# Performance work log

Hardware: AMD Instinct MI355X
Metric: run time of the kernel (lower is better)

## Reference

```python
import jax, jax.numpy as jnp
import numpy as np

B, S, D, H = 4, 2048, 256, 8
HD = D // H
SCALE = float(np.sqrt(HD))  # temperature = head_dim ** 0.5


def setup_inputs() -> dict:
    key = jax.random.key(0)
    ks = jax.random.split(key, 12)
    w = lambda k, shape: jax.random.normal(k, shape, dtype=jnp.float32) * 0.05
    x = jax.random.normal(ks[0], (B, S, D), dtype=jnp.float32)
    adj = jax.random.randint(ks[1], (B, S, S), 0, 2, dtype=jnp.int32)
    return {
        "x": x,
        "adj": adj,
        "w_qkv": w(ks[2], (3 * D, D)),
        "b_qkv": jnp.zeros((3 * D,), jnp.float32),
        "ln_g": jnp.ones((D,), jnp.float32),
        "ln_b": jnp.zeros((D,), jnp.float32),
        "w_fc": w(ks[3], (D, D)),
        "b_fc": jnp.zeros((D,), jnp.float32),
        "w_z": w(ks[4], (D, D)),
        "b_z": jnp.full((D,), -2.0, jnp.float32),  # init_bias fills w_z bias with -2
        "u_z": w(ks[5], (D, D)),
        "w_r": w(ks[6], (D, D)),
        "u_r": w(ks[7], (D, D)),
        "w_g": w(ks[8], (D, D)),
        "u_g": w(ks[9], (D, D)),
    }


def reference(x, adj, w_qkv, b_qkv, ln_g, ln_b, w_fc, b_fc,
              w_z, b_z, u_z, w_r, u_r, w_g, u_g):
    residual = x
    # LayerNorm (eps=1e-5, torch default)
    mu = jnp.mean(x, axis=-1, keepdims=True)
    var = jnp.var(x, axis=-1, keepdims=True)
    xn = (x - mu) / jnp.sqrt(var + 1e-5) * ln_g + ln_b
    # fused QKV projection -> (B*H, S, 3*HD), batch-major over (b, h)
    qkv = xn @ w_qkv.T + b_qkv                       # [B,S,3D]
    qkv = qkv.reshape(B, S, H, 3 * HD).transpose(0, 2, 1, 3).reshape(B * H, S, 3 * HD)
    q, k, v = jnp.split(qkv, 3, axis=-1)
    # masked scaled dot-product attention (full NxN scores, as in original)
    attn = jnp.einsum('nqd,nkd->nqk', q, k) / SCALE  # [B*H,S,S]
    adj_r = jnp.repeat(adj, H, axis=0)               # batch-major, matches attn layout
    attn = jnp.where(adj_r == 0, -jnp.inf, attn)
    attn = jax.nn.softmax(attn, axis=-1)
    out = jnp.einsum('nqk,nkd->nqd', attn, v)        # [B*H,S,HD]
    # Faithful replication of torch's view(n_head, batch, ...) applied to
    # batch-major data (an ordering quirk in the original module).
    out = out.reshape(H, B, S, HD).transpose(1, 2, 0, 3).reshape(B, S, D)
    y = jax.nn.relu(out @ w_fc.T + b_fc)
    # GRU gate: x=residual, y=attention branch
    z = jax.nn.sigmoid(y @ w_z.T + b_z + residual @ u_z.T)
    r = jax.nn.sigmoid(y @ w_r.T + residual @ u_r.T)
    h_hat = jnp.tanh(y @ w_g.T + (r * residual) @ u_g.T)
    return (1.0 - z) * residual + z * h_hat
```

## Files before the change

### kernel.cpp

```cpp
#include <hip/hip_runtime.h>
#include <hip/hip_bf16.h>
#include <math.h>

#define B_  4
#define S_  2048
#define D_  256
#define H_  8
#define HD_ 32
#define QSCALE 0.25504175929589786f

typedef short  bf16x8 __attribute__((ext_vector_type(8)));
typedef float  f32x4  __attribute__((ext_vector_type(4)));
typedef float  f32x16 __attribute__((ext_vector_type(16)));
typedef unsigned short ushort_t;
typedef unsigned int   uint_t;

__device__ __forceinline__ ushort_t f2b(float f) {
    union { float f; unsigned u; } v; v.f = f;
    unsigned r = (v.u + 0x7FFFu + ((v.u >> 16) & 1u)) >> 16;
    return (ushort_t)r;
}
__device__ __forceinline__ float b2f(ushort_t s) {
    return __uint_as_float((uint_t)s << 16);
}
__device__ __forceinline__ f32x16 zero16() {
    f32x16 z;
#pragma unroll
    for (int i = 0; i < 16; ++i) z[i] = 0.f;
    return z;
}

__device__ __forceinline__ float wave_sum(float v) {
#pragma unroll
    for (int o = 32; o > 0; o >>= 1) v += __shfl_down(v, o, 64);
    return v;
}
__device__ __forceinline__ float block_sum256(float v, float* scr) {
    v = wave_sum(v);
    int lane = threadIdx.x & 63, wid = threadIdx.x >> 6;
    if (lane == 0) scr[wid] = v;
    __syncthreads();
    float r = scr[0] + scr[1] + scr[2] + scr[3];
    __syncthreads();
    return r;
}

#define WQ_SZ 196608
#define WS_SZ 65536
#define NB_ADJ 8192
#define NB_WC  2560
#define NB_LN  8192
__global__ __launch_bounds__(256)
void prep_kernel(const int* __restrict__ adj, uint_t* __restrict__ bits,
                 const float* __restrict__ w0, const float* __restrict__ w1,
                 const float* __restrict__ w2, const float* __restrict__ w3,
                 const float* __restrict__ w4, const float* __restrict__ w5,
                 const float* __restrict__ w6, const float* __restrict__ w7,
                 ushort_t* __restrict__ wout,
                 const float* __restrict__ x, const float* __restrict__ g,
                 const float* __restrict__ bb, ushort_t* __restrict__ xn_b) {
    __shared__ float scr[4];
    int blk = blockIdx.x, tid = threadIdx.x;
    if (blk < NB_ADJ) {
        int lane = tid & 63;
#pragma unroll
        for (int gp = 0; gp < 8; ++gp) {
            size_t i = ((size_t)blk * 8 + gp) * 256 + tid;
            unsigned long long m = __ballot(adj[i] != 0);
            size_t wbase = (((size_t)blk * 8 + gp) * 256 + (tid & ~63)) >> 5;
            if (lane == 0)  bits[wbase]     = (uint_t)m;
            if (lane == 32) bits[wbase + 1] = (uint_t)(m >> 32);
        }
    } else if (blk < NB_ADJ + NB_WC) {
        int idx = (blk - NB_ADJ) * 256 + tid;
        const float* src; int o;
        if (idx < WQ_SZ) { src = w0; o = idx; }
        else {
            int j = idx - WQ_SZ, seg = j >> 16; o = j & (WS_SZ - 1);
            src = (seg == 0) ? w1 : (seg == 1) ? w2 : (seg == 2) ? w3 :
                  (seg == 3) ? w4 : (seg == 4) ? w5 : (seg == 5) ? w6 : w7;
        }
        int j  = o & 7;
        int l  = (o >> 3) & 15;
        int qd = (o >> 7) & 3;
        int ks = (o >> 9) & 7;
        int ct = o >> 12;
        wout[idx] = f2b(src[(ct * 16 + l) * 256 + ks * 32 + qd * 8 + j]);
    } else {
        size_t base = (size_t)(blk - NB_ADJ - NB_WC) * D_;
        float v  = x[base + tid];
        float mu = block_sum256(v, scr) * (1.0f / D_);
        float d  = v - mu;
        float var = block_sum256(d * d, scr) * (1.0f / D_);
        float rstd = rsqrtf(var + 1e-5f);
        xn_b[base + tid] = f2b(d * rstd * g[tid] + bb[tid]);
    }
}

__global__ __launch_bounds__(256)
void gemm_qkv(const ushort_t* __restrict__ A, const ushort_t* __restrict__ Wf,
              const float* __restrict__ bias, ushort_t* __restrict__ outb,
              ushort_t* __restrict__ vT) {
    __shared__ ushort_t Sa[64][264];
    int tid = threadIdx.x;
    int wave = tid >> 6, lane = tid & 63, l = lane & 15, quad = lane >> 4;
    int wm = wave >> 1, wn = wave & 1;
    int m0 = blockIdx.y * 64, n0 = blockIdx.x * 64;
    {
        int row = tid >> 2, c0 = (tid & 3) * 64;
        const ushort_t* ap = A + (size_t)(m0 + row) * 256 + c0;
#pragma unroll
        for (int j = 0; j < 8; ++j)
            *(uint4*)&Sa[row][c0 + 8 * j] = ((const uint4*)ap)[j];
    }
    __syncthreads();

    bf16x8 af[2][8];
#pragma unroll
    for (int mt = 0; mt < 2; ++mt)
#pragma unroll
        for (int ks = 0; ks < 8; ++ks)
            af[mt][ks] = *(const bf16x8*)&Sa[wm * 32 + mt * 16 + l][ks * 32 + quad * 8];

    f32x4 acc[2][2];
#pragma unroll
    for (int i = 0; i < 2; ++i)
#pragma unroll
        for (int j = 0; j < 2; ++j) acc[i][j] = (f32x4){0.f, 0.f, 0.f, 0.f};

#pragma unroll
    for (int nt = 0; nt < 2; ++nt) {
        int ct = (n0 >> 4) + wn * 2 + nt;
        bf16x8 wfr[8];
#pragma unroll
        for (int ks = 0; ks < 8; ++ks)
            wfr[ks] = *(const bf16x8*)(Wf + (((size_t)ct * 8 + ks) * 64 + lane) * 8);
#pragma unroll
        for (int ks = 0; ks < 8; ++ks) {
            acc[0][nt] = __builtin_amdgcn_mfma_f32_16x16x32_bf16(af[0][ks], wfr[ks], acc[0][nt], 0, 0, 0);
            acc[1][nt] = __builtin_amdgcn_mfma_f32_16x16x32_bf16(af[1][ks], wfr[ks], acc[1][nt], 0, 0, 0);
        }
    }

    __syncthreads();
    ushort_t* So = &Sa[0][0];
#pragma unroll
    for (int nt = 0; nt < 2; ++nt) {
        int col = wn * 32 + nt * 16 + l;
        int gcol = n0 + col;
        float bv = bias[gcol];
        float qs = ((gcol % 96) < 32) ? QSCALE : 1.0f;
#pragma unroll
        for (int mt = 0; mt < 2; ++mt)
#pragma unroll
            for (int r = 0; r < 4; ++r) {
                int row = wm * 32 + mt * 16 + quad * 4 + r;
                So[row * 72 + col] = f2b((acc[mt][nt][r] + bv) * qs);
            }
    }
    __syncthreads();
    {
        int row = tid >> 2, seg = tid & 3;
        uint4 v0 = *(uint4*)&So[row * 72 + seg * 16];
        uint4 v1 = *(uint4*)&So[row * 72 + seg * 16 + 8];
        ushort_t* op = outb + (size_t)(m0 + row) * 768 + n0 + seg * 16;
        ((uint4*)op)[0] = v0;
        ((uint4*)op)[1] = v1;
    }

    int vs = n0 % 96;
    if (vs != 0) {
        int vloc = (vs == 64) ? 0 : 32;
        int h  = (n0 + vloc) / 96;
        int b  = m0 >> 11;
        int s0 = m0 & (S_ - 1);
        ushort_t* vstage = &Sa[0][0] + 8192;
        {
            int c = tid & 31, seg = tid >> 5;
            ushort_t tmp[8];
#pragma unroll
            for (int i = 0; i < 8; ++i)
                tmp[i] = So[(seg * 8 + i) * 72 + vloc + c];
            uint_t u[4];
#pragma unroll
            for (int i = 0; i < 4; ++i)
                u[i] = (uint_t)tmp[2 * i] | ((uint_t)tmp[2 * i + 1] << 16);
            *(uint4*)&vstage[c * 72 + seg * 8] = make_uint4(u[0], u[1], u[2], u[3]);
        }
        __syncthreads();
        {
            int d = tid >> 3, tseg = tid & 7;
            uint4 v = *(uint4*)&vstage[d * 72 + tseg * 8];
            *(uint4*)&vT[((size_t)(b * 8 + h) * 32 + d) * S_ + s0 + tseg * 8] = v;
        }
    }
}

__global__ __launch_bounds__(256)
void fused_gate(const ushort_t* __restrict__ attn_b, const float* __restrict__ xf,
                const ushort_t* __restrict__ wfc, const ushort_t* __restrict__ wz,
                const ushort_t* __restrict__ uz, const ushort_t* __restrict__ wr,
                const ushort_t* __restrict__ ur, const ushort_t* __restrict__ wg,
                const ushort_t* __restrict__ ug, const float* __restrict__ bfc,
                const float* __restrict__ bz, float* __restrict__ out) {
    __shared__ ushort_t Sa[16][264];
    __shared__ ushort_t Sx[16][264];
    __shared__ ushort_t Sy[16][264];
    __shared__ ushort_t St[16][264];
    int tid = threadIdx.x;
    int wave = tid >> 6, lane = tid & 63, l = lane & 15, quad = lane >> 4;
    int m0 = blockIdx.x * 16;
    int colbase = wave * 64;

    {
        int row = tid >> 4, c0 = (tid & 15) * 16;
        const ushort_t* ap = attn_b + (size_t)(m0 + row) * 256 + c0;
        uint4 a0 = ((const uint4*)ap)[0];
        uint4 a1 = ((const uint4*)ap)[1];
        *(uint4*)&Sa[row][c0] = a0;
        *(uint4*)&Sa[row][c0 + 8] = a1;
        const float4* xp = (const float4*)(xf + (size_t)(m0 + row) * 256 + c0);
        float4 f0 = xp[0], f1 = xp[1], f2_ = xp[2], f3 = xp[3];
        union { __hip_bfloat162 h[4]; uint4 u; } p0, p1;
        p0.h[0] = __float22bfloat162_rn(make_float2(f0.x, f0.y));
        p0.h[1] = __float22bfloat162_rn(make_float2(f0.z, f0.w));
        p0.h[2] = __float22bfloat162_rn(make_float2(f1.x, f1.y));
        p0.h[3] = __float22bfloat162_rn(make_float2(f1.z, f1.w));
        p1.h[0] = __float22bfloat162_rn(make_float2(f2_.x, f2_.y));
        p1.h[1] = __float22bfloat162_rn(make_float2(f2_.z, f2_.w));
        p1.h[2] = __float22bfloat162_rn(make_float2(f3.x, f3.y));
        p1.h[3] = __float22bfloat162_rn(make_float2(f3.z, f3.w));
        *(uint4*)&Sx[row][c0]     = p0.u;
        *(uint4*)&Sx[row][c0 + 8] = p1.u;
    }
    __syncthreads();

    {
        bf16x8 af[8];
#pragma unroll
        for (int ks = 0; ks < 8; ++ks)
            af[ks] = *(const bf16x8*)&Sa[l][ks * 32 + quad * 8];
        f32x4 ya[4];
#pragma unroll
        for (int nt = 0; nt < 4; ++nt) ya[nt] = (f32x4){0.f, 0.f, 0.f, 0.f};
#pragma unroll
        for (int nt = 0; nt < 4; ++nt) {
            size_t fb = ((size_t)(wave * 4 + nt) * 8) * 512 + lane * 8;
#pragma unroll
            for (int ks = 0; ks < 8; ++ks) {
                bf16x8 wfr = *(const bf16x8*)(wfc + fb + ks * 512);
                ya[nt] = __builtin_amdgcn_mfma_f32_16x16x32_bf16(af[ks], wfr, ya[nt], 0, 0, 0);
            }
        }
#pragma unroll
        for (int nt = 0; nt < 4; ++nt) {
            int col = colbase + nt * 16 + l;
            float bv = bfc[col];
#pragma unroll
            for (int r = 0; r < 4; ++r)
                Sy[quad * 4 + r][col] = f2b(fmaxf(ya[nt][r] + bv, 0.0f));
        }
    }
    __syncthreads();

    f32x4 az[4], ar[4], ag[4];
#pragma unroll
    for (int nt = 0; nt < 4; ++nt) {
        az[nt] = (f32x4){0.f, 0.f, 0.f, 0.f};
        ar[nt] = (f32x4){0.f, 0.f, 0.f, 0.f};
        ag[nt] = (f32x4){0.f, 0.f, 0.f, 0.f};
    }
#pragma unroll
    for (int nt = 0; nt < 4; ++nt) {
        size_t fb = ((size_t)(wave * 4 + nt) * 8) * 512 + lane * 8;
#pragma unroll
        for (int ks = 0; ks < 8; ++ks) {
            bf16x8 fy = *(const bf16x8*)&Sy[l][ks * 32 + quad * 8];
            bf16x8 fx = *(const bf16x8*)&Sx[l][ks * 32 + quad * 8];
            bf16x8 fz  = *(const bf16x8*)(wz + fb + ks * 512);
            bf16x8 fuz = *(const bf16x8*)(uz + fb + ks * 512);
            bf16x8 fr  = *(const bf16x8*)(wr + fb + ks * 512);
            bf16x8 fur = *(const bf16x8*)(ur + fb + ks * 512);
            bf16x8 fg  = *(const bf16x8*)(wg + fb + ks * 512);
            az[nt] = __builtin_amdgcn_mfma_f32_16x16x32_bf16(fy, fz,  az[nt], 0, 0, 0);
            az[nt] = __builtin_amdgcn_mfma_f32_16x16x32_bf16(fx, fuz, az[nt], 0, 0, 0);
            ar[nt] = __builtin_amdgcn_mfma_f32_16x16x32_bf16(fy, fr,  ar[nt], 0, 0, 0);
            ar[nt] = __builtin_amdgcn_mfma_f32_16x16x32_bf16(fx, fur, ar[nt], 0, 0, 0);
            ag[nt] = __builtin_amdgcn_mfma_f32_16x16x32_bf16(fy, fg,  ag[nt], 0, 0, 0);
        }
    }
#pragma unroll
    for (int nt = 0; nt < 4; ++nt) {
        int col = colbase + nt * 16 + l;
        float bzv = bz[col];
#pragma unroll
        for (int r = 0; r < 4; ++r) {
            int row = quad * 4 + r;
            az[nt][r] = 1.0f / (1.0f + __expf(-(az[nt][r] + bzv)));
            float rr  = 1.0f / (1.0f + __expf(-ar[nt][r]));
            St[row][col] = f2b(rr * b2f(Sx[row][col]));
        }
    }
    __syncthreads();

    f32x4 fcc[4];
#pragma unroll
    for (int nt = 0; nt < 4; ++nt) fcc[nt] = (f32x4){0.f, 0.f, 0.f, 0.f};
#pragma unroll
    for (int nt = 0; nt < 4; ++nt) {
        size_t fb = ((size_t)(wave * 4 + nt) * 8) * 512 + lane * 8;
#pragma unroll
        for (int ks = 0; ks < 8; ++ks) {
            bf16x8 ft = *(const bf16x8*)&St[l][ks * 32 + quad * 8];
            bf16x8 fu = *(const bf16x8*)(ug + fb + ks * 512);
            fcc[nt] = __builtin_amdgcn_mfma_f32_16x16x32_bf16(ft, fu, fcc[nt], 0, 0, 0);
        }
    }
#pragma unroll
    for (int nt = 0; nt < 4; ++nt) {
        int col = colbase + nt * 16 + l;
#pragma unroll
        for (int r = 0; r < 4; ++r) {
            int row = quad * 4 + r;
            float v = ag[nt][r] + fcc[nt][r];
            float e = __expf(2.0f * v);
            float h = 1.0f - 2.0f / (e + 1.0f);
            float zz = az[nt][r];
            size_t idx = (size_t)(m0 + row) * 256 + col;
            out[idx] = (1.0f - zz) * xf[idx] + zz * h;
        }
    }
}

__global__ __launch_bounds__(256)
void attn_kernel(const ushort_t* __restrict__ qkvb, const ushort_t* __restrict__ vT,
                 const uint_t* __restrict__ abits, ushort_t* __restrict__ attn_b) {
    __shared__ ushort_t Ks[2][64][40];
    __shared__ ushort_t Vt[2][32][72];

    int tid = threadIdx.x;
    int wave = tid >> 6, lane = tid & 63;
    int lane5 = lane & 31, hi = lane >> 5;
    int hsh8 = hi * 8;

    int lid = blockIdx.y * 16 + blockIdx.x;
    int L   = (lid & 7) * 64 + (lid >> 3);
    int q0  = (L & 15) * 128;
    int n   = L >> 4;
    int b = n >> 3, h = n & 7;
    int bp = n & 3, hp = n >> 2;

    const ushort_t* base = qkvb + (size_t)b * S_ * 768 + h * 96;
    int qbase = wave * 32;
    int myq = q0 + qbase + lane5;

    bf16x8 qf1 = *(const bf16x8*)(base + (size_t)myq * 768 + hsh8);
    bf16x8 qf2 = *(const bf16x8*)(base + (size_t)myq * 768 + 16 + hsh8);

    bf16x8 ones;
#pragma unroll
    for (int i = 0; i < 8; ++i) ones[i] = (short)0x3F80;

    f32x16 oacc = zero16(), aones = zero16();

    int skey = tid >> 2, spart = tid & 3;
    int prow = (skey & ~12) | ((skey & 4) << 1) | ((skey & 8) >> 1);
    int kcol = (spart * 8) ^ (((prow >> 3) & 1) << 3);
    int vd = tid >> 3, vk = (tid & 7) * 8;
    const ushort_t* vptr = vT + ((size_t)n * 32 + vd) * S_ + vk;
    const uint_t* aptr = abits + ((size_t)b * S_ + myq) * 64;

    uint2 aw = *(const uint2*)aptr;
    {
        uint4 k0v = *(const uint4*)(base + (size_t)skey * 768 + 32 + spart * 8);
        uint4 v0v = *(const uint4*)(vptr);
        *(uint4*)&Ks[0][prow][kcol] = k0v;
        *(uint4*)&Vt[0][vd][vk] = v0v;
    }
    uint4 kv = *(const uint4*)(base + (size_t)(64 + skey) * 768 + 32 + spart * 8);
    uint4 vv = *(const uint4*)(vptr + 64);
    __syncthreads();

    int b3 = (lane >> 3) & 1;

    for (int k0 = 0; k0 < S_; k0 += 64) {
        int cur = (k0 >> 6) & 1;
        bool more = (k0 + 64 < S_);
        uint2 awn;
        if (more) {
            *(uint4*)&Ks[cur ^ 1][prow][kcol] = kv;
            *(uint4*)&Vt[cur ^ 1][vd][vk] = vv;
            awn = *(const uint2*)(aptr + ((k0 + 64) >> 5));
            if (k0 + 128 < S_) {
                kv = *(const uint4*)(base + (size_t)(k0 + 128 + skey) * 768 + 32 + spart * 8);
                vv = *(const uint4*)(vptr + k0 + 128);
            }
        }
        uint_t awx = aw.x, awy = aw.y;

#pragma unroll
        for (int kb2 = 0; kb2 < 2; ++kb2) {
            const int kb = kb2 * 32;
            bf16x8 kf1 = *(const bf16x8*)&Ks[cur][kb + lane5][(hi ^ b3) * 8];
            bf16x8 kf2 = *(const bf16x8*)&Ks[cur][kb + lane5][((2 + hi) ^ b3) * 8];
            f32x16 sc = zero16();
            sc = __builtin_amdgcn_mfma_f32_32x32x16_bf16(kf1, qf1, sc, 0, 0, 0);
            sc = __builtin_amdgcn_mfma_f32_32x32x16_bf16(kf2, qf2, sc, 0, 0, 0);

            uint_t wsub = (kb2 ? awy : awx) >> hsh8;
            union { uint_t u[8]; bf16x8 v[2]; } pp;
#pragma unroll
            for (int i = 0; i < 8; ++i) {
                const int c = 2 * i + ((i >> 2) * 8);
                float e0 = exp2f(sc[2 * i]);
                float e1 = exp2f(sc[2 * i + 1]);
                uint_t m0 = (uint_t)((int)(wsub << (31 - c)) >> 31);
                uint_t m1 = (uint_t)((int)(wsub << (30 - c)) >> 31);
                e0 = __uint_as_float(__float_as_uint(e0) & m0);
                e1 = __uint_as_float(__float_as_uint(e1) & m1);
                union { __hip_bfloat162 b2; uint_t u; } p;
                p.b2 = __float22bfloat162_rn(make_float2(e0, e1));
                pp.u[i] = p.u;
            }

            bf16x8 vb1 = *(const bf16x8*)&Vt[cur][lane5][kb + hsh8];
            bf16x8 vb2 = *(const bf16x8*)&Vt[cur][lane5][kb + 16 + hsh8];

            __builtin_amdgcn_s_setprio(1);
            oacc  = __builtin_amdgcn_mfma_f32_32x32x16_bf16(pp.v[0], vb1,  oacc,  0, 0, 0);
            aones = __builtin_amdgcn_mfma_f32_32x32x16_bf16(pp.v[0], ones, aones, 0, 0, 0);
            oacc  = __builtin_amdgcn_mfma_f32_32x32x16_bf16(pp.v[1], vb2,  oacc,  0, 0, 0);
            aones = __builtin_amdgcn_mfma_f32_32x32x16_bf16(pp.v[1], ones, aones, 0, 0, 0);
            __builtin_amdgcn_s_setprio(0);
        }

        if (more) aw = awn;
        __syncthreads();
    }

    ushort_t* Ost = &Ks[0][0][0];
#pragma unroll
    for (int r = 0; r < 16; ++r) {
        int qr = (r & 3) + 8 * (r >> 2) + 4 * hi;
        Ost[(qbase + qr) * 40 + lane5] = f2b(oacc[r] / aones[r]);
    }
    __syncthreads();
#pragma unroll
    for (int bt = 0; bt < 2; ++bt) {
        int row = (tid >> 2) + bt * 64;
        int part = tid & 3;
        uint4 v = *(uint4*)&Ost[row * 40 + part * 8];
        *(uint4*)&attn_b[((size_t)(bp * S_ + q0 + row)) * 256 + hp * 32 + part * 8] = v;
    }
}

extern "C" void kernel_launch(void* const* d_in, const int* in_sizes, int n_in,
                              void* d_out, int out_size, void* d_ws, size_t ws_size,
                              hipStream_t stream) {
    const float* x     = (const float*)d_in[0];
    const int*   adj   = (const int*)d_in[1];
    const float* w_qkv = (const float*)d_in[2];
    const float* b_qkv = (const float*)d_in[3];
    const float* ln_g  = (const float*)d_in[4];
    const float* ln_b  = (const float*)d_in[5];
    const float* w_fc  = (const float*)d_in[6];
    const float* b_fc  = (const float*)d_in[7];
    const float* w_z   = (const float*)d_in[8];
    const float* b_z   = (const float*)d_in[9];
    const float* u_z   = (const float*)d_in[10];
    const float* w_r   = (const float*)d_in[11];
    const float* u_r   = (const float*)d_in[12];
    const float* w_g   = (const float*)d_in[13];
    const float* u_g   = (const float*)d_in[14];
    float* out = (float*)d_out;

    const size_t TOK  = (size_t)B_ * S_;
    const size_t TOKD = TOK * D_;
    ushort_t* xn_b   = (ushort_t*)d_ws;
    ushort_t* qkv_b  = xn_b + TOKD;
    ushort_t* attn_b = qkv_b + TOK * 768;
    ushort_t* wb     = attn_b + TOKD;
    uint_t*   bits   = (uint_t*)(wb + WQ_SZ + 7 * WS_SZ);
    ushort_t* vTb    = (ushort_t*)(bits + (size_t)B_ * S_ * S_ / 32);

    ushort_t* wq_b  = wb;
    ushort_t* wfc_b = wb + WQ_SZ;
    ushort_t* wz_b  = wfc_b + WS_SZ;
    ushort_t* uz_b  = wz_b + WS_SZ;
    ushort_t* wr_b  = uz_b + WS_SZ;
    ushort_t* ur_b  = wr_b + WS_SZ;
    ushort_t* wg_b  = ur_b + WS_SZ;
    ushort_t* ug_b  = wg_b + WS_SZ;

    prep_kernel<<<NB_ADJ + NB_WC + NB_LN, 256, 0, stream>>>(
        adj, bits, w_qkv, w_fc, w_z, u_z, w_r, u_r, w_g, u_g, wb,
        x, ln_g, ln_b, xn_b);

    gemm_qkv<<<dim3(12, 128), 256, 0, stream>>>(xn_b, wq_b, b_qkv, qkv_b, vTb);

    attn_kernel<<<dim3(S_ / 128, B_ * H_), 256, 0, stream>>>(qkv_b, vTb, bits, attn_b);

    fused_gate<<<512, 256, 0, stream>>>(
        attn_b, x, wfc_b, wz_b, uz_b, wr_b, ur_b, wg_b, ug_b, b_fc, b_z, out);
}
```

Before: 235.9 us.

## Split key tile across wave pairs in attention and reduce partial accumulators

The attention kernel now gives each block 64 queries instead of 128 and doubles the grid. Each pair of waves shares a 32-query tile, and each wave in the pair handles one 32-key half of every 64-key tile. The two partial output and denominator accumulators are summed through shared memory at the end. This raises parallelism and occupancy and shortens each wave's serial loop, at the cost of K/V tiles being loaded once per 64 queries instead of per 128, plus an extra LDS reduction with barriers.

```diff
diff --git a/kernel.cpp b/kernel.cpp
--- a/kernel.cpp
+++ b/kernel.cpp
@@ -342,17 +342,19 @@
     int wave = tid >> 6, lane = tid & 63;
     int lane5 = lane & 31, hi = lane >> 5;
     int hsh8 = hi * 8;
-
-    int lid = blockIdx.y * 16 + blockIdx.x;
-    int L   = (lid & 7) * 64 + (lid >> 3);
-    int q0  = (L & 15) * 128;
-    int n   = L >> 4;
+    int pair = wave >> 1, half = wave & 1;
+
+    int lid = blockIdx.y * 32 + blockIdx.x;
+    int L   = (lid & 7) * 128 + (lid >> 3);
+    int q0  = (L & 31) * 64;
+    int n   = L >> 5;
     int b = n >> 3, h = n & 7;
     int bp = n & 3, hp = n >> 2;
 
     const ushort_t* base = qkvb + (size_t)b * S_ * 768 + h * 96;
-    int qbase = wave * 32;
+    int qbase = pair * 32;
     int myq = q0 + qbase + lane5;
+    const int kb = half * 32;
 
     bf16x8 qf1 = *(const bf16x8*)(base + (size_t)myq * 768 + hsh8);
     bf16x8 qf2 = *(const bf16x8*)(base + (size_t)myq * 768 + 16 + hsh8);
@@ -368,9 +370,9 @@
     int kcol = (spart * 8) ^ (((prow >> 3) & 1) << 3);
     int vd = tid >> 3, vk = (tid & 7) * 8;
     const ushort_t* vptr = vT + ((size_t)n * 32 + vd) * S_ + vk;
-    const uint_t* aptr = abits + ((size_t)b * S_ + myq) * 64;
-
-    uint2 aw = *(const uint2*)aptr;
+    const uint_t* aptr = abits + ((size_t)b * S_ + myq) * 64 + half;
+
+    uint_t aw = aptr[0];
     {
         uint4 k0v = *(const uint4*)(base + (size_t)skey * 768 + 32 + spart * 8);
         uint4 v0v = *(const uint4*)(vptr);
@@ -386,69 +388,100 @@
     for (int k0 = 0; k0 < S_; k0 += 64) {
         int cur = (k0 >> 6) & 1;
         bool more = (k0 + 64 < S_);
-        uint2 awn;
+        uint_t awn;
         if (more) {
             *(uint4*)&Ks[cur ^ 1][prow][kcol] = kv;
             *(uint4*)&Vt[cur ^ 1][vd][vk] = vv;
-            awn = *(const uint2*)(aptr + ((k0 + 64) >> 5));
+            awn = aptr[(k0 + 64) >> 5];
             if (k0 + 128 < S_) {
                 kv = *(const uint4*)(base + (size_t)(k0 + 128 + skey) * 768 + 32 + spart * 8);
                 vv = *(const uint4*)(vptr + k0 + 128);
             }
         }
-        uint_t awx = aw.x, awy = aw.y;
-
-#pragma unroll
-        for (int kb2 = 0; kb2 < 2; ++kb2) {
-            const int kb = kb2 * 32;
-            bf16x8 kf1 = *(const bf16x8*)&Ks[cur][kb + lane5][(hi ^ b3) * 8];
-            bf16x8 kf2 = *(const bf16x8*)&Ks[cur][kb + lane5][((2 + hi) ^ b3) * 8];
-            f32x16 sc = zero16();
-            sc = __builtin_amdgcn_mfma_f32_32x32x16_bf16(kf1, qf1, sc, 0, 0, 0);
-            sc = __builtin_amdgcn_mfma_f32_32x32x16_bf16(kf2, qf2, sc, 0, 0, 0);
-
-            uint_t wsub = (kb2 ? awy : awx) >> hsh8;
-            union { uint_t u[8]; bf16x8 v[2]; } pp;
-#pragma unroll
-            for (int i = 0; i < 8; ++i) {
-                const int c = 2 * i + ((i >> 2) * 8);
-                float e0 = exp2f(sc[2 * i]);
-                float e1 = exp2f(sc[2 * i + 1]);
-                uint_t m0 = (uint_t)((int)(wsub << (31 - c)) >> 31);
-                uint_t m1 = (uint_t)((int)(wsub << (30 - c)) >> 31);
-                e0 = __uint_as_float(__float_as_uint(e0) & m0);
-                e1 = __uint_as_float(__float_as_uint(e1) & m1);
-                union { __hip_bfloat162 b2; uint_t u; } p;
-                p.b2 = __float22bfloat162_rn(make_float2(e0, e1));
-                pp.u[i] = p.u;
-            }
-
-            bf16x8 vb1 = *(const bf16x8*)&Vt[cur][lane5][kb + hsh8];
-            bf16x8 vb2 = *(const bf16x8*)&Vt[cur][lane5][kb + 16 + hsh8];
-
-            __builtin_amdgcn_s_setprio(1);
-            oacc  = __builtin_amdgcn_mfma_f32_32x32x16_bf16(pp.v[0], vb1,  oacc,  0, 0, 0);
-            aones = __builtin_amdgcn_mfma_f32_32x32x16_bf16(pp.v[0], ones, aones, 0, 0, 0);
-            oacc  = __builtin_amdgcn_mfma_f32_32x32x16_bf16(pp.v[1], vb2,  oacc,  0, 0, 0);
-            aones = __builtin_amdgcn_mfma_f32_32x32x16_bf16(pp.v[1], ones, aones, 0, 0, 0);
-            __builtin_amdgcn_s_setprio(0);
-        }
+
+        bf16x8 kf1 = *(const bf16x8*)&Ks[cur][kb + lane5][(hi ^ b3) * 8];
+        bf16x8 kf2 = *(const bf16x8*)&Ks[cur][kb + lane5][((2 + hi) ^ b3) * 8];
+        f32x16 sc = zero16();
+        sc = __builtin_amdgcn_mfma_f32_32x32x16_bf16(kf1, qf1, sc, 0, 0, 0);
+        sc = __builtin_amdgcn_mfma_f32_32x32x16_bf16(kf2, qf2, sc, 0, 0, 0);
+
+        uint_t wsub = aw >> hsh8;
+        union { uint_t u[8]; bf16x8 v[2]; } pp;
+#pragma unroll
+        for (int i = 0; i < 8; ++i) {
+            const int c = 2 * i + ((i >> 2) * 8);
+            float e0 = exp2f(sc[2 * i]);
+            float e1 = exp2f(sc[2 * i + 1]);
+            uint_t m0 = (uint_t)((int)(wsub << (31 - c)) >> 31);
+            uint_t m1 = (uint_t)((int)(wsub << (30 - c)) >> 31);
+            e0 = __uint_as_float(__float_as_uint(e0) & m0);
+            e1 = __uint_as_float(__float_as_uint(e1) & m1);
+            union { __hip_bfloat162 b2; uint_t u; } p;
+            p.b2 = __float22bfloat162_rn(make_float2(e0, e1));
+            pp.u[i] = p.u;
+        }
+
+        bf16x8 vb1 = *(const bf16x8*)&Vt[cur][lane5][kb + hsh8];
+        bf16x8 vb2 = *(const bf16x8*)&Vt[cur][lane5][kb + 16 + hsh8];
+
+        __builtin_amdgcn_s_setprio(1);
+        oacc  = __builtin_amdgcn_mfma_f32_32x32x16_bf16(pp.v[0], vb1,  oacc,  0, 0, 0);
+        aones = __builtin_amdgcn_mfma_f32_32x32x16_bf16(pp.v[0], ones, aones, 0, 0, 0);
+        oacc  = __builtin_amdgcn_mfma_f32_32x32x16_bf16(pp.v[1], vb2,  oacc,  0, 0, 0);
+        aones = __builtin_amdgcn_mfma_f32_32x32x16_bf16(pp.v[1], ones, aones, 0, 0, 0);
+        __builtin_amdgcn_s_setprio(0);
 
         if (more) aw = awn;
         __syncthreads();
     }
 
+    float* red = (float*)&Ks[0][0][0];
+    if (half) {
+        float* dst = red + pair * 2048 + lane * 4;
+#pragma unroll
+        for (int j = 0; j < 4; ++j) {
+            f32x4 t;
+            t[0] = oacc[4 * j]; t[1] = oacc[4 * j + 1];
+            t[2] = oacc[4 * j + 2]; t[3] = oacc[4 * j + 3];
+            *(f32x4*)(dst + j * 256) = t;
+        }
+#pragma unroll
+        for (int j = 0; j < 4; ++j) {
+            f32x4 t;
+            t[0] = aones[4 * j]; t[1] = aones[4 * j + 1];
+            t[2] = aones[4 * j + 2]; t[3] = aones[4 * j + 3];
+            *(f32x4*)(dst + (4 + j) * 256) = t;
+        }
+    }
+    __syncthreads();
+    if (!half) {
+        const float* src = red + pair * 2048 + lane * 4;
+#pragma unroll
+        for (int j = 0; j < 4; ++j) {
+            f32x4 t = *(const f32x4*)(src + j * 256);
+            oacc[4 * j] += t[0]; oacc[4 * j + 1] += t[1];
+            oacc[4 * j + 2] += t[2]; oacc[4 * j + 3] += t[3];
+        }
+#pragma unroll
+        for (int j = 0; j < 4; ++j) {
+            f32x4 t = *(const f32x4*)(src + (4 + j) * 256);
+            aones[4 * j] += t[0]; aones[4 * j + 1] += t[1];
+            aones[4 * j + 2] += t[2]; aones[4 * j + 3] += t[3];
+        }
+    }
+    __syncthreads();
+
     ushort_t* Ost = &Ks[0][0][0];
-#pragma unroll
-    for (int r = 0; r < 16; ++r) {
-        int qr = (r & 3) + 8 * (r >> 2) + 4 * hi;
-        Ost[(qbase + qr) * 40 + lane5] = f2b(oacc[r] / aones[r]);
-    }
-    __syncthreads();
-#pragma unroll
-    for (int bt = 0; bt < 2; ++bt) {
-        int row = (tid >> 2) + bt * 64;
-        int part = tid & 3;
+    if (!half) {
+#pragma unroll
+        for (int r = 0; r < 16; ++r) {
+            int qr = (r & 3) + 8 * (r >> 2) + 4 * hi;
+            Ost[(qbase + qr) * 40 + lane5] = f2b(oacc[r] / aones[r]);
+        }
+    }
+    __syncthreads();
+    {
+        int row = tid >> 2, part = tid & 3;
         uint4 v = *(uint4*)&Ost[row * 40 + part * 8];
         *(uint4*)&attn_b[((size_t)(bp * S_ + q0 + row)) * 256 + hp * 32 + part * 8] = v;
     }
@@ -498,7 +531,7 @@
 
     gemm_qkv<<<dim3(12, 128), 256, 0, stream>>>(xn_b, wq_b, b_qkv, qkv_b, vTb);
 
-    attn_kernel<<<dim3(S_ / 128, B_ * H_), 256, 0, stream>>>(qkv_b, vTb, bits, attn_b);
+    attn_kernel<<<dim3(S_ / 64, B_ * H_), 256, 0, stream>>>(qkv_b, vTb, bits, attn_b);
 
     fused_gate<<<512, 256, 0, stream>>>(
         attn_b, x, wfc_b, wz_b, uz_b, wr_b, ur_b, wg_b, ug_b, b_fc, b_z, out);
```

Result: no change. 236.5 us (+0.3%).
